# Kernel tuning notes

Measured on AMD Instinct MI355X. Metric: run time of the kernel, lower is better.

Reference implementation:

```python
import jax, jax.numpy as jnp
import numpy as np

DEPTH, HEADS, DIM, DHEAD, MLP = 4, 16, 1024, 64, 4096
B, N, M = 4, 1024, 1024
EPS = 1e-5


def layer_norm(x, w, b):
    mu = jnp.mean(x, axis=-1, keepdims=True)
    var = jnp.var(x, axis=-1, keepdims=True)
    return (x - mu) * jax.lax.rsqrt(var + EPS) * w + b


def setup_inputs() -> dict:
    key = jax.random.key(0)
    ks = jax.random.split(key, 16)
    inner = HEADS * DHEAD
    s = lambda fan_in: 1.0 / np.sqrt(fan_in)
    # weights stored in (in, out) layout: y = x @ W + b
    return {
        "x": jax.random.normal(ks[0], (B, N, DIM), jnp.float32),
        "m": jax.random.normal(ks[1], (B, M, DIM), jnp.float32),
        "Wq": jax.random.normal(ks[2], (DEPTH, DIM, inner), jnp.float32) * s(DIM),
        "Wk": jax.random.normal(ks[3], (DEPTH, DIM, inner), jnp.float32) * s(DIM),
        "Wv": jax.random.normal(ks[4], (DEPTH, DIM, inner), jnp.float32) * s(DIM),
        "Wo": jax.random.normal(ks[5], (DEPTH, inner, DIM), jnp.float32) * s(inner),
        "bo": jnp.zeros((DEPTH, DIM), jnp.float32),
        "ln1_w": jnp.ones((DEPTH, DIM), jnp.float32),
        "ln1_b": jnp.zeros((DEPTH, DIM), jnp.float32),
        "W1": jax.random.normal(ks[6], (DEPTH, DIM, MLP), jnp.float32) * s(DIM),
        "b1": jnp.zeros((DEPTH, MLP), jnp.float32),
        "W2": jax.random.normal(ks[7], (DEPTH, MLP, DIM), jnp.float32) * s(MLP),
        "b2": jnp.zeros((DEPTH, DIM), jnp.float32),
        "ln2_w": jnp.ones((DEPTH, DIM), jnp.float32),
        "ln2_b": jnp.zeros((DEPTH, DIM), jnp.float32),
    }


def reference(x, m, Wq, Wk, Wv, Wo, bo, ln1_w, ln1_b, W1, b1, W2, b2, ln2_w, ln2_b):
    scale = DIM ** (-0.5)  # NOTE: original scales by dim**-0.5, not dim_head**-0.5
    for i in range(DEPTH):
        # cross-attention block (PreNorm on x only; m is used raw, as in source)
        h = layer_norm(x, ln1_w[i], ln1_b[i])
        q = jnp.einsum('bnd,de->bne', h, Wq[i]).reshape(B, N, HEADS, DHEAD)
        k = jnp.einsum('bmd,de->bme', m, Wk[i]).reshape(B, M, HEADS, DHEAD)
        v = jnp.einsum('bmd,de->bme', m, Wv[i]).reshape(B, M, HEADS, DHEAD)
        dots = jnp.einsum('bihd,bjhd->bhij', q, k) * scale
        attn = jax.nn.softmax(dots, axis=-1)
        out = jnp.einsum('bhij,bjhd->bihd', attn, v).reshape(B, N, HEADS * DHEAD)
        x = x + jnp.einsum('bne,ed->bnd', out, Wo[i]) + bo[i]
        # feed-forward block
        h2 = layer_norm(x, ln2_w[i], ln2_b[i])
        ff = jax.nn.gelu(jnp.einsum('bnd,df->bnf', h2, W1[i]) + b1[i], approximate=False)
        x = x + jnp.einsum('bnf,fd->bnd', ff, W2[i]) + b2[i]
    return x
```

## Files before the change

### kernel.cpp

```cpp
#include <hip/hip_runtime.h>
#include <hip/hip_bf16.h>
#include <math.h>

typedef __hip_bfloat16 bf16;
typedef __attribute__((ext_vector_type(8))) short bf16x8;
typedef __attribute__((ext_vector_type(4))) float f32x4;

#define DEPTH  4
#define HEADS  16
#define DIM    1024
#define DHEAD  64
#define MLPD   4096
#define BB     4
#define NN     1024
#define MMK    1024
#define ROWS   (BB*NN)
#define QKVS   3072

__device__ inline float bitsbf(short s) {
  union { float f; unsigned u; } c; c.u = ((unsigned)(unsigned short)s) << 16; return c.f;
}
__device__ inline short bfbits(float f) {
  bf16 h = __float2bfloat16(f); return *(short*)&h;
}

__device__ inline void gload_lds16(const bf16* g, bf16* l) {
  __builtin_amdgcn_global_load_lds((const __attribute__((address_space(1))) unsigned int*)g,
                                   (__attribute__((address_space(3))) unsigned int*)l, 16, 0, 0);
}

__global__ __launch_bounds__(256) void f2b_kernel(const float* __restrict__ in, bf16* __restrict__ out, int n) {
  int i = blockIdx.x * 256 + threadIdx.x;
  if (i < n) out[i] = __float2bfloat16(in[i]);
}

__global__ __launch_bounds__(256) void transpose_f2b(const float* __restrict__ in, bf16* __restrict__ out,
                                                     int inStride, int rowOff, int colOff, int outStride) {
  __shared__ float tile[32][33];
  int n0 = blockIdx.x * 32, k0 = blockIdx.y * 32;
  int tx = threadIdx.x, ty = threadIdx.y;
  #pragma unroll
  for (int i = 0; i < 32; i += 8)
    tile[ty + i][tx] = in[(size_t)(rowOff + k0 + ty + i) * inStride + colOff + n0 + tx];
  __syncthreads();
  #pragma unroll
  for (int i = 0; i < 32; i += 8)
    out[(size_t)(n0 + ty + i) * outStride + k0 + tx] = __float2bfloat16(tile[tx][ty + i]);
}

__global__ __launch_bounds__(256) void ln_kernel(const float* __restrict__ x, const float* __restrict__ w,
                                                 const float* __restrict__ b, bf16* __restrict__ out) {
  int row = blockIdx.x, t = threadIdx.x;
  const float* xr = x + (size_t)row * DIM;
  float4 xv = *(const float4*)(xr + t * 4);
  float s  = xv.x + xv.y + xv.z + xv.w;
  float s2 = xv.x * xv.x + xv.y * xv.y + xv.z * xv.z + xv.w * xv.w;
  #pragma unroll
  for (int off = 32; off; off >>= 1) { s += __shfl_xor(s, off, 64); s2 += __shfl_xor(s2, off, 64); }
  __shared__ float sh_s[4], sh_s2[4], sh_mu, sh_rstd;
  int wid = t >> 6;
  if ((t & 63) == 0) { sh_s[wid] = s; sh_s2[wid] = s2; }
  __syncthreads();
  if (t == 0) {
    float S1 = sh_s[0] + sh_s[1] + sh_s[2] + sh_s[3];
    float S2 = sh_s2[0] + sh_s2[1] + sh_s2[2] + sh_s2[3];
    float mu = S1 * (1.0f / DIM);
    float var = S2 * (1.0f / DIM) - mu * mu;
    sh_mu = mu; sh_rstd = rsqrtf(var + 1e-5f);
  }
  __syncthreads();
  float mu = sh_mu, rstd = sh_rstd;
  float4 wv = *(const float4*)(w + t * 4);
  float4 bv = *(const float4*)(b + t * 4);
  bf16* orow = out + (size_t)row * DIM + t * 4;
  orow[0] = __float2bfloat16((xv.x - mu) * rstd * wv.x + bv.x);
  orow[1] = __float2bfloat16((xv.y - mu) * rstd * wv.y + bv.y);
  orow[2] = __float2bfloat16((xv.z - mu) * rstd * wv.z + bv.z);
  orow[3] = __float2bfloat16((xv.w - mu) * rstd * wv.w + bv.w);
}

#define MODE_PLAIN 0
#define MODE_GELU  1
#define MODE_RES   2
#define BM 128
#define BK 32

template<int JT>
__global__ __launch_bounds__(256) void gemm_tile(const bf16* __restrict__ A, const bf16* __restrict__ Bt,
                                                 const float* __restrict__ bias, bf16* __restrict__ outb,
                                                 float* __restrict__ resf, int outStride, int K, int mode) {
  constexpr int BN = JT * 32;
  __shared__ __align__(16) bf16 As[2][BM * BK];
  __shared__ __align__(16) bf16 Bs[2][BN * BK];
  int t = threadIdx.x;
  int w = t >> 6, l = t & 63;
  int l15 = l & 15, quad = l >> 4;
  int col0 = blockIdx.x * BN, row0 = blockIdx.y * BM;
  int wm = (w >> 1) * 64, wn = (w & 1) * (JT * 16);

  f32x4 acc[4][JT] = {};

  int sm = w * 16 + (l >> 2);
  int sk = (l & 3) * 8;
  const bf16* ag0 = A  + (size_t)(row0 + sm) * K + sk;
  const bf16* ag1 = A  + (size_t)(row0 + 64 + sm) * K + sk;
  const bf16* bg0 = Bt + (size_t)(col0 + sm) * K + sk;
  const bf16* bg1 = Bt + (size_t)(col0 + 64 + sm) * K + sk;

  gload_lds16(ag0, &As[0][w * 512]);
  gload_lds16(ag1, &As[0][2048 + w * 512]);
  gload_lds16(bg0, &Bs[0][w * 512]);
  if constexpr (JT == 4) gload_lds16(bg1, &Bs[0][2048 + w * 512]);

  int cur = 0;
  for (int k0 = 0; k0 < K; k0 += BK) {
    __syncthreads();
    int nxt = cur ^ 1;
    if (k0 + BK < K) {
      gload_lds16(ag0 + k0 + BK, &As[nxt][w * 512]);
      gload_lds16(ag1 + k0 + BK, &As[nxt][2048 + w * 512]);
      gload_lds16(bg0 + k0 + BK, &Bs[nxt][w * 512]);
      if constexpr (JT == 4) gload_lds16(bg1 + k0 + BK, &Bs[nxt][2048 + w * 512]);
    }
    bf16x8 af[4], bfr[JT];
    #pragma unroll
    for (int i = 0; i < 4; ++i)  af[i]  = *(const bf16x8*)&As[cur][(wm + i * 16 + l15) * BK + quad * 8];
    #pragma unroll
    for (int j = 0; j < JT; ++j) bfr[j] = *(const bf16x8*)&Bs[cur][(wn + j * 16 + l15) * BK + quad * 8];
    #pragma unroll
    for (int i = 0; i < 4; ++i)
      #pragma unroll
      for (int j = 0; j < JT; ++j)
        acc[i][j] = __builtin_amdgcn_mfma_f32_16x16x32_bf16(af[i], bfr[j], acc[i][j], 0, 0, 0);
    cur = nxt;
  }

  #pragma unroll
  for (int i = 0; i < 4; ++i) {
    #pragma unroll
    for (int j = 0; j < JT; ++j) {
      int gcol = col0 + wn + j * 16 + l15;
      float bval = (mode != MODE_PLAIN && bias != nullptr) ? bias[gcol] : 0.0f;
      #pragma unroll
      for (int r = 0; r < 4; ++r) {
        int grow = row0 + wm + i * 16 + quad * 4 + r;
        float val = acc[i][j][r];
        size_t idx = (size_t)grow * outStride + gcol;
        if (mode == MODE_RES) {
          resf[idx] = resf[idx] + val + bval;
        } else {
          if (mode == MODE_GELU) {
            float u = val + bval;
            val = 0.5f * u * (1.0f + erff(u * 0.70710678118654752f));
          }
          outb[idx] = __float2bfloat16(val);
        }
      }
    }
  }
}

#define ALDP 72

__global__ __launch_bounds__(256) void attn_mfma_kernel(const bf16* __restrict__ qkv, bf16* __restrict__ o) {
  __shared__ __align__(16) short Kl[64][ALDP];
  __shared__ __align__(16) short Vt[64][ALDP];
  __shared__ __align__(16) short Pl[64][ALDP];

  int t = threadIdx.x;
  int lane = t & 63, w = t >> 6;
  int l15 = lane & 15, quad = lane >> 4;
  int bh = blockIdx.x;
  int qt = blockIdx.y;
  int b = bh >> 4, hh = bh & 15;

  const bf16* q = qkv;
  const bf16* k = qkv + 1024;
  const bf16* v = qkv + 2048;

  bf16x8 qfrag[2];
  {
    const bf16* qp = q + (size_t)(b * NN + qt * 64 + w * 16 + l15) * QKVS + hh * DHEAD + quad * 8;
    #pragma unroll
    for (int ks = 0; ks < 2; ++ks) {
      bf16x8 raw = *(const bf16x8*)(qp + ks * 32);
      bf16x8 sc;
      #pragma unroll
      for (int e = 0; e < 8; ++e) sc[e] = bfbits(bitsbf(raw[e]) * 0.03125f);
      qfrag[ks] = sc;
    }
  }

  f32x4 Oacc[4] = {{}, {}, {}, {}};
  float mrow[4] = {-1e30f, -1e30f, -1e30f, -1e30f};
  float lrow[4] = {0.f, 0.f, 0.f, 0.f};

  int srow = t >> 2, sc0 = (t & 3) * 16;

  for (int kt = 0; kt < MMK / 64; ++kt) {
    __syncthreads();
    {
      const bf16* kp = k + (size_t)(b * MMK + kt * 64 + srow) * QKVS + hh * DHEAD + sc0;
      *(bf16x8*)&Kl[srow][sc0]     = *(const bf16x8*)kp;
      *(bf16x8*)&Kl[srow][sc0 + 8] = *(const bf16x8*)(kp + 8);
      const bf16* vp = v + (size_t)(b * MMK + kt * 64 + srow) * QKVS + hh * DHEAD + sc0;
      bf16x8 v0 = *(const bf16x8*)vp;
      bf16x8 v1 = *(const bf16x8*)(vp + 8);
      #pragma unroll
      for (int e = 0; e < 8; ++e) {
        Vt[sc0 + e][srow]     = v0[e];
        Vt[sc0 + 8 + e][srow] = v1[e];
      }
    }
    __syncthreads();

    f32x4 S[4] = {{}, {}, {}, {}};
    #pragma unroll
    for (int ks = 0; ks < 2; ++ks) {
      #pragma unroll
      for (int j = 0; j < 4; ++j) {
        bf16x8 bfr = *(const bf16x8*)&Kl[j * 16 + l15][ks * 32 + quad * 8];
        S[j] = __builtin_amdgcn_mfma_f32_16x16x32_bf16(qfrag[ks], bfr, S[j], 0, 0, 0);
      }
    }

    #pragma unroll
    for (int r = 0; r < 4; ++r) {
      float tm = fmaxf(fmaxf(S[0][r], S[1][r]), fmaxf(S[2][r], S[3][r]));
      tm = fmaxf(tm, __shfl_xor(tm, 1, 64));
      tm = fmaxf(tm, __shfl_xor(tm, 2, 64));
      tm = fmaxf(tm, __shfl_xor(tm, 4, 64));
      tm = fmaxf(tm, __shfl_xor(tm, 8, 64));
      float mn = fmaxf(mrow[r], tm);
      float alpha = __expf(mrow[r] - mn);
      mrow[r] = mn;
      float rs = 0.f;
      #pragma unroll
      for (int j = 0; j < 4; ++j) {
        float p = __expf(S[j][r] - mn);
        S[j][r] = p;
        rs += p;
      }
      rs += __shfl_xor(rs, 1, 64);
      rs += __shfl_xor(rs, 2, 64);
      rs += __shfl_xor(rs, 4, 64);
      rs += __shfl_xor(rs, 8, 64);
      lrow[r] = lrow[r] * alpha + rs;
      #pragma unroll
      for (int j = 0; j < 4; ++j) {
        Oacc[j][r] *= alpha;
        Pl[w * 16 + quad * 4 + r][j * 16 + l15] = bfbits(S[j][r]);
      }
    }
    __syncthreads();

    #pragma unroll
    for (int ks = 0; ks < 2; ++ks) {
      bf16x8 pa = *(const bf16x8*)&Pl[w * 16 + l15][ks * 32 + quad * 8];
      #pragma unroll
      for (int j = 0; j < 4; ++j) {
        bf16x8 vb = *(const bf16x8*)&Vt[j * 16 + l15][ks * 32 + quad * 8];
        Oacc[j] = __builtin_amdgcn_mfma_f32_16x16x32_bf16(pa, vb, Oacc[j], 0, 0, 0);
      }
    }
  }

  #pragma unroll
  for (int r = 0; r < 4; ++r) {
    float inv = 1.0f / lrow[r];
    bf16* op = o + (size_t)(b * NN + qt * 64 + w * 16 + quad * 4 + r) * DIM + hh * DHEAD;
    #pragma unroll
    for (int j = 0; j < 4; ++j)
      op[j * 16 + l15] = __float2bfloat16(Oacc[j][r] * inv);
  }
}

extern "C" void kernel_launch(void* const* d_in, const int* in_sizes, int n_in,
                              void* d_out, int out_size, void* d_ws, size_t ws_size,
                              hipStream_t stream) {
  const float* x_in = (const float*)d_in[0];
  const float* m    = (const float*)d_in[1];
  const float* Wq   = (const float*)d_in[2];
  const float* Wk   = (const float*)d_in[3];
  const float* Wv   = (const float*)d_in[4];
  const float* Wo   = (const float*)d_in[5];
  const float* bo   = (const float*)d_in[6];
  const float* ln1w = (const float*)d_in[7];
  const float* ln1b = (const float*)d_in[8];
  const float* W1   = (const float*)d_in[9];
  const float* b1   = (const float*)d_in[10];
  const float* W2   = (const float*)d_in[11];
  const float* b2   = (const float*)d_in[12];
  const float* ln2w = (const float*)d_in[13];
  const float* ln2b = (const float*)d_in[14];

  float* xf = (float*)d_out;

  char* ws = (char*)d_ws;
  bf16* h    = (bf16*)(ws + 0);
  bf16* mb   = (bf16*)(ws + (8u  << 20));
  bf16* qkv  = (bf16*)(ws + (16u << 20));
  bf16* ffh  = (bf16*)(ws + (16u << 20));
  bf16* wt   = (bf16*)(ws + (40u << 20));

  const int NTOK = ROWS * DIM;

  hipMemcpyAsync(xf, x_in, (size_t)NTOK * sizeof(float), hipMemcpyDeviceToDevice, stream);
  f2b_kernel<<<dim3((NTOK + 255) / 256), dim3(256), 0, stream>>>(m, mb, NTOK);

  dim3 blk(256);
  dim3 tblk(32, 8);
  dim3 g_n1(DIM / 64, ROWS / BM);
  dim3 g_n2(2048 / 128, ROWS / BM);
  dim3 tr_1k(DIM / 32, DIM / 32);
  dim3 tr_w1(2048 / 32, DIM / 32);
  dim3 tr_w2(DIM / 32, 2048 / 32);
  dim3 attn_grid(BB * HEADS, NN / 64);

  for (int L = 0; L < DEPTH; ++L) {
    const float* WqL = Wq + (size_t)L * DIM * DIM;
    const float* WkL = Wk + (size_t)L * DIM * DIM;
    const float* WvL = Wv + (size_t)L * DIM * DIM;
    const float* WoL = Wo + (size_t)L * DIM * DIM;
    const float* W1L = W1 + (size_t)L * DIM * MLPD;
    const float* W2L = W2 + (size_t)L * MLPD * DIM;

    ln_kernel<<<dim3(ROWS), blk, 0, stream>>>(xf, ln1w + L * DIM, ln1b + L * DIM, h);

    transpose_f2b<<<tr_1k, tblk, 0, stream>>>(WkL, wt, DIM, 0, 0, DIM);
    transpose_f2b<<<tr_1k, tblk, 0, stream>>>(WvL, wt + 1024 * 1024, DIM, 0, 0, DIM);
    gemm_tile<4><<<g_n2, blk, 0, stream>>>(mb, wt, nullptr, qkv + 1024, nullptr, QKVS, DIM, MODE_PLAIN);

    transpose_f2b<<<tr_1k, tblk, 0, stream>>>(WqL, wt, DIM, 0, 0, DIM);
    gemm_tile<2><<<g_n1, blk, 0, stream>>>(h, wt, nullptr, qkv, nullptr, QKVS, DIM, MODE_PLAIN);

    attn_mfma_kernel<<<attn_grid, blk, 0, stream>>>(qkv, h);

    transpose_f2b<<<tr_1k, tblk, 0, stream>>>(WoL, wt, DIM, 0, 0, DIM);
    gemm_tile<2><<<g_n1, blk, 0, stream>>>(h, wt, bo + L * DIM, nullptr, xf, DIM, DIM, MODE_RES);

    ln_kernel<<<dim3(ROWS), blk, 0, stream>>>(xf, ln2w + L * DIM, ln2b + L * DIM, h);

    for (int half = 0; half < 2; ++half) {
      transpose_f2b<<<tr_w1, tblk, 0, stream>>>(W1L, wt, MLPD, 0, half * 2048, DIM);
      gemm_tile<4><<<g_n2, blk, 0, stream>>>(h, wt, b1 + (size_t)L * MLPD + half * 2048, ffh, nullptr,
                                             2048, DIM, MODE_GELU);
      transpose_f2b<<<tr_w2, tblk, 0, stream>>>(W2L, wt, DIM, half * 2048, 0, 2048);
      gemm_tile<2><<<g_n1, blk, 0, stream>>>(ffh, wt, (half == 0) ? (b2 + (size_t)L * DIM) : nullptr,
                                             nullptr, xf, DIM, 2048, MODE_RES);
    }
  }
}
```

Measured before the change: 1.695 ms.

## Double-buffer attention K/V tiles with async LDS loads and widen GEMM tiles

Restructures the attention kernel to double-buffer K and V tiles in shared memory. K is loaded directly to LDS via gload_lds16 with an XOR-swizzled layout, and the next V tile is prefetched into registers, so global loads overlap with MFMA work and one barrier per iteration is removed. Separately, the 1024-wide GEMMs switch from the 64-column tile variant to the 128-column variant. The risks are a possible race on the P buffer now that the barrier before PV is gone, higher LDS use, and fewer blocks for the 1K-wide GEMMs.

```diff
diff --git a/kernel.cpp b/kernel.cpp
--- a/kernel.cpp
+++ b/kernel.cpp
@@ -163,8 +163,8 @@
 #define ALDP 72
 
 __global__ __launch_bounds__(256) void attn_mfma_kernel(const bf16* __restrict__ qkv, bf16* __restrict__ o) {
-  __shared__ __align__(16) short Kl[64][ALDP];
-  __shared__ __align__(16) short Vt[64][ALDP];
+  __shared__ __align__(16) bf16  Kl[2][64 * 64];
+  __shared__ __align__(16) short Vt[2][64][ALDP];
   __shared__ __align__(16) short Pl[64][ALDP];
 
   int t = threadIdx.x;
@@ -178,6 +178,14 @@
   const bf16* k = qkv + 1024;
   const bf16* v = qkv + 2048;
 
+  int krow = w * 16 + (lane >> 3);
+  int kcol = ((lane & 7) ^ (lane >> 3)) * 8;
+  const bf16* kg0 = k + (size_t)(b * MMK + krow) * QKVS + hh * DHEAD + kcol;
+  const bf16* kg1 = kg0 + (size_t)8 * QKVS;
+
+  int srow = t >> 2, sc0 = (t & 3) * 16;
+  const bf16* vg = v + (size_t)(b * MMK + srow) * QKVS + hh * DHEAD + sc0;
+
   bf16x8 qfrag[2];
   {
     const bf16* qp = q + (size_t)(b * NN + qt * 64 + w * 16 + l15) * QKVS + hh * DHEAD + quad * 8;
@@ -191,35 +199,42 @@
     }
   }
 
+  gload_lds16(kg0, &Kl[0][w * 1024]);
+  gload_lds16(kg1, &Kl[0][w * 1024 + 512]);
+  {
+    bf16x8 v0 = *(const bf16x8*)vg;
+    bf16x8 v1 = *(const bf16x8*)(vg + 8);
+    #pragma unroll
+    for (int e = 0; e < 8; ++e) {
+      Vt[0][sc0 + e][srow]     = v0[e];
+      Vt[0][sc0 + 8 + e][srow] = v1[e];
+    }
+  }
+
   f32x4 Oacc[4] = {{}, {}, {}, {}};
   float mrow[4] = {-1e30f, -1e30f, -1e30f, -1e30f};
   float lrow[4] = {0.f, 0.f, 0.f, 0.f};
 
-  int srow = t >> 2, sc0 = (t & 3) * 16;
-
+  int cur = 0;
   for (int kt = 0; kt < MMK / 64; ++kt) {
     __syncthreads();
-    {
-      const bf16* kp = k + (size_t)(b * MMK + kt * 64 + srow) * QKVS + hh * DHEAD + sc0;
-      *(bf16x8*)&Kl[srow][sc0]     = *(const bf16x8*)kp;
-      *(bf16x8*)&Kl[srow][sc0 + 8] = *(const bf16x8*)(kp + 8);
-      const bf16* vp = v + (size_t)(b * MMK + kt * 64 + srow) * QKVS + hh * DHEAD + sc0;
-      bf16x8 v0 = *(const bf16x8*)vp;
-      bf16x8 v1 = *(const bf16x8*)(vp + 8);
-      #pragma unroll
-      for (int e = 0; e < 8; ++e) {
-        Vt[sc0 + e][srow]     = v0[e];
-        Vt[sc0 + 8 + e][srow] = v1[e];
-      }
-    }
-    __syncthreads();
+    int nxt = cur ^ 1;
+    bool more = (kt + 1 < MMK / 64);
+    bf16x8 nv0, nv1;
+    if (more) {
+      const bf16* vgn = vg + (size_t)(kt + 1) * 64 * QKVS;
+      nv0 = *(const bf16x8*)vgn;
+      nv1 = *(const bf16x8*)(vgn + 8);
+      gload_lds16(kg0 + (size_t)(kt + 1) * 64 * QKVS, &Kl[nxt][w * 1024]);
+      gload_lds16(kg1 + (size_t)(kt + 1) * 64 * QKVS, &Kl[nxt][w * 1024 + 512]);
+    }
 
     f32x4 S[4] = {{}, {}, {}, {}};
     #pragma unroll
     for (int ks = 0; ks < 2; ++ks) {
       #pragma unroll
       for (int j = 0; j < 4; ++j) {
-        bf16x8 bfr = *(const bf16x8*)&Kl[j * 16 + l15][ks * 32 + quad * 8];
+        bf16x8 bfr = *(const bf16x8*)&Kl[cur][(j * 16 + l15) * 64 + (((ks * 4 + quad) ^ (l15 & 7)) * 8)];
         S[j] = __builtin_amdgcn_mfma_f32_16x16x32_bf16(qfrag[ks], bfr, S[j], 0, 0, 0);
       }
     }
@@ -252,17 +267,25 @@
         Pl[w * 16 + quad * 4 + r][j * 16 + l15] = bfbits(S[j][r]);
       }
     }
-    __syncthreads();
 
     #pragma unroll
     for (int ks = 0; ks < 2; ++ks) {
       bf16x8 pa = *(const bf16x8*)&Pl[w * 16 + l15][ks * 32 + quad * 8];
       #pragma unroll
       for (int j = 0; j < 4; ++j) {
-        bf16x8 vb = *(const bf16x8*)&Vt[j * 16 + l15][ks * 32 + quad * 8];
+        bf16x8 vb = *(const bf16x8*)&Vt[cur][j * 16 + l15][ks * 32 + quad * 8];
         Oacc[j] = __builtin_amdgcn_mfma_f32_16x16x32_bf16(pa, vb, Oacc[j], 0, 0, 0);
       }
     }
+
+    if (more) {
+      #pragma unroll
+      for (int e = 0; e < 8; ++e) {
+        Vt[nxt][sc0 + e][srow]     = nv0[e];
+        Vt[nxt][sc0 + 8 + e][srow] = nv1[e];
+      }
+    }
+    cur = nxt;
   }
 
   #pragma unroll
@@ -310,8 +333,8 @@
 
   dim3 blk(256);
   dim3 tblk(32, 8);
-  dim3 g_n1(DIM / 64, ROWS / BM);
-  dim3 g_n2(2048 / 128, ROWS / BM);
+  dim3 g_1k(DIM / 128, ROWS / BM);
+  dim3 g_2k(2048 / 128, ROWS / BM);
   dim3 tr_1k(DIM / 32, DIM / 32);
   dim3 tr_w1(2048 / 32, DIM / 32);
   dim3 tr_w2(DIM / 32, 2048 / 32);
@@ -329,24 +352,24 @@
 
     transpose_f2b<<<tr_1k, tblk, 0, stream>>>(WkL, wt, DIM, 0, 0, DIM);
     transpose_f2b<<<tr_1k, tblk, 0, stream>>>(WvL, wt + 1024 * 1024, DIM, 0, 0, DIM);
-    gemm_tile<4><<<g_n2, blk, 0, stream>>>(mb, wt, nullptr, qkv + 1024, nullptr, QKVS, DIM, MODE_PLAIN);
+    gemm_tile<4><<<g_2k, blk, 0, stream>>>(mb, wt, nullptr, qkv + 1024, nullptr, QKVS, DIM, MODE_PLAIN);
 
     transpose_f2b<<<tr_1k, tblk, 0, stream>>>(WqL, wt, DIM, 0, 0, DIM);
-    gemm_tile<2><<<g_n1, blk, 0, stream>>>(h, wt, nullptr, qkv, nullptr, QKVS, DIM, MODE_PLAIN);
+    gemm_tile<4><<<g_1k, blk, 0, stream>>>(h, wt, nullptr, qkv, nullptr, QKVS, DIM, MODE_PLAIN);
 
     attn_mfma_kernel<<<attn_grid, blk, 0, stream>>>(qkv, h);
 
     transpose_f2b<<<tr_1k, tblk, 0, stream>>>(WoL, wt, DIM, 0, 0, DIM);
-    gemm_tile<2><<<g_n1, blk, 0, stream>>>(h, wt, bo + L * DIM, nullptr, xf, DIM, DIM, MODE_RES);
+    gemm_tile<4><<<g_1k, blk, 0, stream>>>(h, wt, bo + L * DIM, nullptr, xf, DIM, DIM, MODE_RES);
 
     ln_kernel<<<dim3(ROWS), blk, 0, stream>>>(xf, ln2w + L * DIM, ln2b + L * DIM, h);
 
     for (int half = 0; half < 2; ++half) {
       transpose_f2b<<<tr_w1, tblk, 0, stream>>>(W1L, wt, MLPD, 0, half * 2048, DIM);
-      gemm_tile<4><<<g_n2, blk, 0, stream>>>(h, wt, b1 + (size_t)L * MLPD + half * 2048, ffh, nullptr,
+      gemm_tile<4><<<g_2k, blk, 0, stream>>>(h, wt, b1 + (size_t)L * MLPD + half * 2048, ffh, nullptr,
                                              2048, DIM, MODE_GELU);
       transpose_f2b<<<tr_w2, tblk, 0, stream>>>(W2L, wt, DIM, half * 2048, 0, 2048);
-      gemm_tile<2><<<g_n1, blk, 0, stream>>>(ffh, wt, (half == 0) ? (b2 + (size_t)L * DIM) : nullptr,
+      gemm_tile<4><<<g_1k, blk, 0, stream>>>(ffh, wt, (half == 0) ? (b2 + (size_t)L * DIM) : nullptr,
                                              nullptr, xf, DIM, 2048, MODE_RES);
     }
   }
```

New measurement: 1.834 ms. 1.08x slower.
